# Kernel optimization log

Hardware: AMD Instinct MI355X
Metric: run time of the kernel (lower is better)

Reference implementation:

```python
import jax, jax.numpy as jnp
import numpy as np

S = 8            # n_internal_streams
N = 2**S - 1     # 255 cliques (all non-empty subsets of streams)
D = 32           # half_dim = consciousness_dim // 2
INPUT_DIM = 512
NUM_ITER = 5
B = 1024


def _configs():
    # binary membership of each clique (non-empty subsets), [N, S]
    return ((np.arange(1, 2**S)[:, None] >> np.arange(S)) & 1).astype(np.float32)


def setup_inputs() -> dict:
    key = jax.random.key(0)
    ks = jax.random.split(key, 10)
    cfg = _configs()
    depths = cfg.sum(-1)
    # topological amplitude init: gaussian profile over clique depth
    center, sigma = S / 2.0, S / 3.0
    prof = np.exp(-((depths - center) ** 2) / (2 * sigma ** 2))
    prof = prof / (np.linalg.norm(prof) + 1e-8)
    psi_A0 = jnp.asarray(np.broadcast_to(prof[None, :, None], (1, N, D)).copy(),
                         jnp.float32) + jax.random.normal(ks[0], (1, N, D)) * 0.01
    inp = {
        'network_state': jax.random.normal(ks[1], (B, INPUT_DIM), jnp.float32),
        'W_streams': jax.random.normal(ks[2], (S * D, INPUT_DIM)) / np.sqrt(INPUT_DIM),
        'b_streams': jnp.zeros((S * D,), jnp.float32),
        'W_A': jax.random.normal(ks[3], (D, D)) / np.sqrt(D),
        'b_A': jnp.zeros((D,), jnp.float32),
        'W_phi': jax.random.normal(ks[4], (D, D)) / np.sqrt(D),
        'b_phi': jnp.zeros((D,), jnp.float32),
        'psi_A0': psi_A0,
        'psi_phi0': jax.random.normal(ks[5], (1, N, D)) * 0.3,
        'W_comp': jax.random.normal(ks[6], (32, N)) / np.sqrt(N),
        'b_comp': jnp.zeros((32,), jnp.float32),
        'W_read': jax.random.normal(ks[7], (2 * D, 32 * D)) / np.sqrt(32 * D),
        'b_read': jnp.zeros((2 * D,), jnp.float32),
        'alpha_kin': jnp.asarray(0.5, jnp.float32),
        'mass_sq': jnp.asarray(0.1, jnp.float32),
        'potential_weight': jnp.asarray(0.3, jnp.float32),
        'input_weight': jnp.asarray(0.5, jnp.float32),
        'evolution_rate': jnp.asarray(0.3, jnp.float32),
        'phase_coupling': jnp.asarray(1.0, jnp.float32),
    }
    return inp


def reference(network_state, W_streams, b_streams, W_A, b_A, W_phi, b_phi,
              psi_A0, psi_phi0, W_comp, b_comp, W_read, b_read,
              alpha_kin, mass_sq, potential_weight, input_weight,
              evolution_rate, phase_coupling):
    cfg = jnp.asarray(_configs())                      # [N,S]
    depths = cfg.sum(-1)                               # [N]
    # Hamming-distance kernel between clique configurations
    Ham = cfg @ (1.0 - cfg).T + (1.0 - cfg) @ cfg.T    # [N,N]
    K = jnp.exp(-Ham / S)
    krow = K.sum(1)                                    # [N]

    Bb = network_state.shape[0]
    feats = (network_state @ W_streams.T + b_streams).reshape(Bb, S, D)
    # clique features: mean of member-stream features
    cf = jnp.einsum('ns,bsd->bnd', cfg, feats) / depths[None, :, None]
    A_input = jax.nn.softplus(cf @ W_A.T + b_A)        # [B,N,D]
    phi_input = jnp.pi * jnp.tanh(cf @ W_phi.T + b_phi)

    A = jax.nn.softplus(jnp.broadcast_to(psi_A0, (Bb, N, D)))
    phi = jnp.broadcast_to(psi_phi0, (Bb, N, D))
    dt = jax.nn.sigmoid(evolution_rate)

    for _ in range(NUM_ITER):
        # laplacian: sum_j K_ij (A_j - A_i) / N  (factorized, same math)
        KA = jnp.einsum('ij,bjd->bid', K, A)
        lap = (KA - krow[None, :, None] * A) / N
        sp, cp = jnp.sin(phi), jnp.cos(phi)
        Ks = jnp.einsum('ij,bjd->bid', K, sp)
        Kc = jnp.einsum('ij,bjd->bid', K, cp)
        # sum_j K_ij A_i sin(phi_j - phi_i) / N
        pc = A * (cp * Ks - sp * Kc) / N
        # nonlocal potential: V_i = sum_j K_ij A_j cos(phi_j - phi_i) / N
        KAc = jnp.einsum('ij,bjd->bid', K, A * cp)
        KAs = jnp.einsum('ij,bjd->bid', K, A * sp)
        V = (cp * KAc + sp * KAs) / N
        input_drive = A_input * jnp.sin(phi_input - phi)
        dA = (alpha_kin * lap + potential_weight * V - mass_sq * A
              + input_weight * (A_input - A))
        A = jax.nn.softplus(A + dt * dA)               # updated A used in dphi
        dphi = alpha_kin * pc / (A + 1e-8) + input_weight * input_drive
        phi = phi + dt * dphi
        # per-clique norm clip to 1
        norms = jnp.maximum(jnp.linalg.norm(A, axis=-1, keepdims=True), 1e-8)
        A = A * jnp.where(norms > 1.0, 1.0 / norms, 1.0)

    A_t = jnp.swapaxes(A, 1, 2)                        # [B,D,N]
    Ac = jax.nn.relu(A_t @ W_comp.T + b_comp)          # [B,D,32]
    ro = Ac.reshape(Bb, -1) @ W_read.T + b_read        # [B,2D]
    amplitude = jax.nn.softplus(ro[:, :D])
    phase = jnp.tanh(ro[:, D:] * phase_coupling) * jnp.pi
    psi = (amplitude * jnp.cos(phase)).astype(jnp.complex64) + 1j * (amplitude * jnp.sin(phase)).astype(jnp.complex64)
    return psi, amplitude, phase
```

## Files before the change

### kernel.cpp

```cpp
#include <hip/hip_runtime.h>
#include <math.h>

#define PI_F   3.14159265358979f
#define QF     0.88249690258459546f
#define INV255 (1.0f/255.0f)

__device__ __forceinline__ float softplus_f(float x){
    return fmaxf(x, 0.0f) + __logf(1.0f + __expf(-fabsf(x)));
}
__device__ __forceinline__ float tanh_fast(float x){
    const float e = __expf(2.0f*x);
    return fmaf(-2.0f, __builtin_amdgcn_rcpf(e + 1.0f), 1.0f);
}

template<int CTRL>
__device__ __forceinline__ float dppmov(float x){
    return __int_as_float(__builtin_amdgcn_mov_dpp(__float_as_int(x), CTRL, 0xF, 0xF, false));
}
__device__ __forceinline__ float lxor1 (float x){ return dppmov<0xB1>(x);  }
__device__ __forceinline__ float lxor2 (float x){ return dppmov<0x4E>(x);  }
__device__ __forceinline__ float lxor8 (float x){ return dppmov<0x128>(x); }
__device__ __forceinline__ float lxor4 (float x){ return __int_as_float(__builtin_amdgcn_ds_swizzle(__float_as_int(x), 0x101F)); }
__device__ __forceinline__ float lxor16(float x){ return __int_as_float(__builtin_amdgcn_ds_swizzle(__float_as_int(x), 0x401F)); }
__device__ __forceinline__ float lxor32(float x){ return __shfl_xor(x, 32, 64); }

template<int CTRL>
__device__ __forceinline__ float dppadd(float v){
    return v + __int_as_float(__builtin_amdgcn_update_dpp(0, __float_as_int(v), CTRL, 0xF, 0xF, true));
}
__device__ __forceinline__ float wave_sum63(float v){
    v = dppadd<0x111>(v);
    v = dppadd<0x112>(v);
    v = dppadd<0x114>(v);
    v = dppadd<0x118>(v);
    v = dppadd<0x142>(v);
    v = dppadd<0x143>(v);
    return v;
}

template<int NA>
__device__ __forceinline__ void bflyN(float (&x)[NA][4]){
    const float qv = QF;
    #pragma unroll
    for (int a = 0; a < NA; a++){
        #pragma unroll
        for (int r = 0; r < 4; r++) x[a][r] = fmaf(lxor1 (x[a][r]), qv, x[a][r]);
    }
    #pragma unroll
    for (int a = 0; a < NA; a++){
        #pragma unroll
        for (int r = 0; r < 4; r++) x[a][r] = fmaf(lxor2 (x[a][r]), qv, x[a][r]);
    }
    #pragma unroll
    for (int a = 0; a < NA; a++){
        #pragma unroll
        for (int r = 0; r < 4; r++) x[a][r] = fmaf(lxor8 (x[a][r]), qv, x[a][r]);
    }
    #pragma unroll
    for (int a = 0; a < NA; a++){
        #pragma unroll
        for (int r = 0; r < 4; r++) x[a][r] = fmaf(lxor4 (x[a][r]), qv, x[a][r]);
    }
    #pragma unroll
    for (int a = 0; a < NA; a++){
        #pragma unroll
        for (int r = 0; r < 4; r++) x[a][r] = fmaf(lxor16(x[a][r]), qv, x[a][r]);
    }
    #pragma unroll
    for (int a = 0; a < NA; a++){
        #pragma unroll
        for (int r = 0; r < 4; r++) x[a][r] = fmaf(lxor32(x[a][r]), qv, x[a][r]);
    }
    #pragma unroll
    for (int a = 0; a < NA; a++){
        float t0 = x[a][0], t2 = x[a][2];
        x[a][0] = fmaf(QF, x[a][1], x[a][0]);
        x[a][1] = fmaf(QF, t0,      x[a][1]);
        x[a][2] = fmaf(QF, x[a][3], x[a][2]);
        x[a][3] = fmaf(QF, t2,      x[a][3]);
        t0 = x[a][0]; float t1 = x[a][1];
        x[a][0] = fmaf(QF, x[a][2], x[a][0]);
        x[a][1] = fmaf(QF, x[a][3], x[a][1]);
        x[a][2] = fmaf(QF, t0,      x[a][2]);
        x[a][3] = fmaf(QF, t1,      x[a][3]);
    }
}

__global__ __launch_bounds__(256) void prep_kernel(
        const float* __restrict__ Ws,    const float* __restrict__ psiA0,
        const float* __restrict__ psiP0, const float* __restrict__ p_alpha,
        const float* __restrict__ p_msq, const float* __restrict__ p_pw,
        const float* __restrict__ p_iw,  const float* __restrict__ p_evo,
        float* __restrict__ WsT,  float* __restrict__ Xc,  float* __restrict__ P0c,
        float* __restrict__ F0c)
{
    if (blockIdx.x < 32){
        __shared__ float tile[64][65];
        const int rt = blockIdx.x & 3, ct = blockIdx.x >> 2;
        const int r0 = rt*64, c0t = ct*64;
        const int tx = threadIdx.x & 63, ty = threadIdx.x >> 6;
        #pragma unroll
        for (int k = 0; k < 16; k++){
            const int row = ty*16 + k;
            tile[row][tx] = Ws[(r0+row)*512 + c0t + tx];
        }
        __syncthreads();
        #pragma unroll
        for (int k = 0; k < 16; k++){
            const int row = ty*16 + k;
            WsT[(c0t+row)*256 + r0 + tx] = tile[tx][row];
        }
        return;
    }
    const int tid = threadIdx.x;
    const int w = tid >> 6, l = tid & 63;
    const float alpha = p_alpha[0], msq = p_msq[0], pw = p_pw[0], iw = p_iw[0];
    const float dt   = 1.0f / (1.0f + __expf(-p_evo[0]));
    const float dta  = dt * alpha * INV255;
    const float dtpw = dt * pw * INV255;
    const float c0   = 1.0f - dt * (msq + iw);
    const float m0 = (l == 0) ? 0.0f : 1.0f;
    int nn[4]; float krow[4];
    float c18;
    { const float t1 = 1.0f + QF, t2 = t1*t1, t4 = t2*t2; c18 = t4*t4; }
    #pragma unroll
    for (int r = 0; r < 4; r++){
        nn[r] = l + 64*r;
        krow[r] = c18 - __expf(-0.125f * (float)__popc(nn[r]));
    }
    #pragma unroll
    for (int dd = 0; dd < 8; dd++){
        const int d = w*8 + dd;
        float A0[4], ph0[4], sp[4], cp[4];
        float x[5][4];
        #pragma unroll
        for (int r = 0; r < 4; r++){
            const int n = nn[r];
            A0[r]  = (n > 0) ? softplus_f(psiA0[(n-1)*32 + d]) : 0.0f;
            ph0[r] = (n > 0) ? psiP0[(n-1)*32 + d] : 0.0f;
            sp[r] = __sinf(ph0[r]); cp[r] = __cosf(ph0[r]);
            const float mk = (r == 0) ? m0 : 1.0f;
            const float xa = A0[r] * mk;
            x[0][r] = xa;
            x[1][r] = sp[r] * mk;
            x[2][r] = cp[r] * mk;
            x[3][r] = xa * cp[r];
            x[4][r] = xa * sp[r];
        }
        bflyN<5>(x);
        #pragma unroll
        for (int r = 0; r < 4; r++){
            const float Ao   = A0[r];
            const float lapp = fmaf(-krow[r], Ao, x[0][r]);
            const float Vp   = fmaf(cp[r], x[3][r], sp[r]*x[4][r]);
            const float Pp   = fmaf(-sp[r], x[2][r], cp[r]*x[1][r]);
            float X = c0 * Ao;
            X = fmaf(dta,  lapp, X);
            X = fmaf(dtpw, Vp,   X);
            const int idx = d*256 + nn[r];
            Xc[idx]  = X;
            P0c[idx] = dta * Ao * Pp;
            F0c[idx] = ph0[r];
        }
    }
}

template<bool USET>
__global__ __launch_bounds__(512, 4) void fused_kernel(
        const float* __restrict__ ns,
        const float* __restrict__ Ws,
        const float* __restrict__ WsT,
        const float* __restrict__ bs,
        const float* __restrict__ WA,
        const float* __restrict__ bA,
        const float* __restrict__ WP,
        const float* __restrict__ bP,
        const float* __restrict__ psiA0,
        const float* __restrict__ psiP0,
        const float* __restrict__ Xc,
        const float* __restrict__ P0c,
        const float* __restrict__ F0c,
        const float* __restrict__ Wcomp,
        const float* __restrict__ bcomp,
        const float* __restrict__ Wread,
        const float* __restrict__ bread,
        const float* __restrict__ p_alpha, const float* __restrict__ p_msq,
        const float* __restrict__ p_pw,    const float* __restrict__ p_iw,
        const float* __restrict__ p_evo,   const float* __restrict__ p_pcpl,
        float* __restrict__ out, int Bb)
{
    __shared__ __align__(16) float2 ST[16][512];
    __shared__ __align__(16) float  red[2048];
    __shared__ __align__(16) float  hA[256];
    __shared__ __align__(16) float  hP[256];
    __shared__ __align__(16) float  nsb[512];
    __shared__ __align__(16) float  fe[256];

    float* ac  = red;
    float* rop = red + 1024;

    const int b   = blockIdx.x;
    const int tid = threadIdx.x;
    const int w   = tid >> 6, l = tid & 63;

    const float alpha = p_alpha[0], msq = p_msq[0], pw = p_pw[0], iw = p_iw[0];
    const float pcpl  = p_pcpl[0];
    const float dt    = 1.0f / (1.0f + __expf(-p_evo[0]));
    const float dta  = dt * alpha * INV255;
    const float dtpw = dt * pw * INV255;
    const float c0   = 1.0f - dt * (msq + iw);
    const float dtiw = dt * iw;

    nsb[tid] = ns[b*512 + tid];
    __syncthreads();
    {
        const int k = tid >> 1, part = tid & 1;
        float f = (part == 0) ? bs[k] : 0.0f;
        if (USET){
            const float4* nb4 = (const float4*)nsb + part*64;
            const float*  colb = WsT + (part*64)*1024 + k;
            #pragma unroll 8
            for (int j4 = 0; j4 < 64; j4++){
                const float4 nv = nb4[j4];
                const float* col = colb + j4*1024;
                f = fmaf(col[0],   nv.x, f);
                f = fmaf(col[256], nv.y, f);
                f = fmaf(col[512], nv.z, f);
                f = fmaf(col[768], nv.w, f);
            }
        } else {
            const float4* wr  = (const float4*)(Ws + k*512) + part*64;
            const float4* nb4 = (const float4*)nsb + part*64;
            #pragma unroll 8
            for (int i = 0; i < 64; i++){
                const float4 wv = wr[i], nv = nb4[i];
                f = fmaf(wv.x, nv.x, f); f = fmaf(wv.y, nv.y, f);
                f = fmaf(wv.z, nv.z, f); f = fmaf(wv.w, nv.w, f);
            }
        }
        red[part*256 + k] = f;
    }
    __syncthreads();
    if (tid < 256) fe[tid] = red[tid] + red[256 + tid];
    __syncthreads();
    {
        const int t2 = tid & 255;
        const int s = t2 >> 5, d2 = t2 & 31;
        const float* Wm = (tid < 256) ? WA : WP;
        float acc = 0.0f;
        #pragma unroll 8
        for (int dp = 0; dp < 32; dp++)
            acc = fmaf(Wm[d2*32 + dp], fe[s*32 + dp], acc);
        if (tid < 256) hA[t2] = acc; else hP[t2] = acc;
    }
    __syncthreads();

    int   nn[4];
    float krow[4];
    const float m0 = (l == 0) ? 0.0f : 1.0f;
    float c18;
    { const float t1 = 1.0f + QF, t2 = t1*t1, t4 = t2*t2; c18 = t4*t4; }
    #pragma unroll
    for (int r = 0; r < 4; r++){
        nn[r] = l + 64*r;
        krow[r] = c18 - __expf(-0.125f * (float)__popc(nn[r]));
    }

    float CAp[4][4], Dsp[4][4], Dcp[4][4];
    float scl_c[4] = {1.0f, 1.0f, 1.0f, 1.0f};
    float nrm0[4] = {0.f, 0.f, 0.f, 0.f};

    #pragma unroll
    for (int dd = 0; dd < 4; dd++){
        const int d = w*4 + dd;
        const float bAd = bA[d], bPd = bP[d];
        float gA_[8], gP_[8];
        #pragma unroll
        for (int s = 0; s < 8; s++){ gA_[s] = hA[s*32 + d]; gP_[s] = hP[s*32 + d]; }
        #pragma unroll
        for (int r = 0; r < 4; r++){
            const int pop = __popc(nn[r]);
            const float rdep = 1.0f / (float)(pop ? pop : 1);
            float sA = 0.0f, sP = 0.0f;
            #pragma unroll
            for (int s = 0; s < 8; s++){
                if ((nn[r] >> s) & 1){ sA += gA_[s]; sP += gP_[s]; }
            }
            const float uA  = fmaf(sA, rdep, bAd);
            const float uP  = fmaf(sP, rdep, bPd);
            const float Ain = softplus_f(uA);
            const float pin = PI_F * tanh_fast(uP);
            const float ca = dtiw * Ain;
            CAp[dd][r] = ca;
            Dsp[dd][r] = ca * __sinf(pin);
            Dcp[dd][r] = ca * __cosf(pin);
            if (USET){
                const int idx = d*256 + nn[r];
                const float An = softplus_f(Xc[idx] + ca);
                const float rr = __builtin_amdgcn_rcpf(An + 1e-8f);
                const float F0 = F0c[idx];
                float pb = fmaf(ca, __sinf(pin - F0), F0);
                ST[dd*4 + r][tid] = make_float2(An, fmaf(P0c[idx], rr, pb));
                nrm0[r] = fmaf(An, An, nrm0[r]);
            } else {
                const int nm1 = (nn[r] > 0) ? (nn[r] - 1) : 0;
                ST[dd*4 + r][tid] = make_float2(softplus_f(psiA0[nm1*32 + d]),
                                                psiP0[nm1*32 + d]);
            }
        }
        __builtin_amdgcn_sched_barrier(0);
    }

    if (USET){
        #pragma unroll
        for (int r = 0; r < 4; r++) red[w*256 + nn[r]] = nrm0[r];
        __syncthreads();
        #pragma unroll
        for (int r = 0; r < 4; r++){
            const int n = nn[r];
            const float t = red[n]        + red[256 + n]  + red[512 + n]  + red[768 + n]
                          + red[1024 + n] + red[1280 + n] + red[1536 + n] + red[1792 + n];
            scl_c[r] = (t > 1.0f) ? rsqrtf(t) : 1.0f;
        }
        __syncthreads();
    }

    float2 stn[4];
    #pragma unroll
    for (int r = 0; r < 4; r++) stn[r] = ST[r][tid];

    const int NFULL = USET ? 3 : 4;
    for (int it = 0; it < NFULL; it++){
        float nrm[4] = {0.f, 0.f, 0.f, 0.f};
        #pragma unroll
        for (int dd = 0; dd < 4; dd++){
            float Al[4], ph[4], sp[4], cp[4];
            #pragma unroll
            for (int r = 0; r < 4; r++){
                Al[r] = stn[r].x * scl_c[r];
                ph[r] = stn[r].y;
            }
            if (dd < 3){
                #pragma unroll
                for (int r = 0; r < 4; r++) stn[r] = ST[(dd+1)*4 + r][tid];
            }
            float x[5][4];
            {
                sp[0] = __sinf(ph[0]); cp[0] = __cosf(ph[0]);
                const float xa = Al[0] * m0;
                x[0][0] = xa;
                x[1][0] = sp[0] * m0;
                x[2][0] = cp[0] * m0;
                x[3][0] = xa * cp[0];
                x[4][0] = xa * sp[0];
            }
            #pragma unroll
            for (int r = 1; r < 4; r++){
                sp[r] = __sinf(ph[r]); cp[r] = __cosf(ph[r]);
                const float xa = Al[r];
                x[0][r] = xa;
                x[1][r] = sp[r];
                x[2][r] = cp[r];
                x[3][r] = xa * cp[r];
                x[4][r] = xa * sp[r];
            }
            bflyN<5>(x);
            #pragma unroll
            for (int r = 0; r < 4; r++){
                const float Ao   = Al[r];
                const float lapp = fmaf(-krow[r], Ao, x[0][r]);
                const float Vp   = fmaf(cp[r], x[3][r], sp[r]*x[4][r]);
                float Aarg = fmaf(c0, Ao, CAp[dd][r]);
                Aarg = fmaf(dta,  lapp, Aarg);
                Aarg = fmaf(dtpw, Vp,   Aarg);
                const float An = softplus_f(Aarg);
                const float Pp = fmaf(-sp[r], x[2][r], cp[r]*x[1][r]);
                const float rr = __builtin_amdgcn_rcpf(An + 1e-8f);
                float pb = fmaf(Dsp[dd][r], cp[r], ph[r]);
                pb = fmaf(-Dcp[dd][r], sp[r], pb);
                ST[dd*4 + r][tid] = make_float2(An, fmaf(dta*Ao, Pp*rr, pb));
                nrm[r] = fmaf(An, An, nrm[r]);
            }
            __builtin_amdgcn_sched_barrier(0);
        }
        #pragma unroll
        for (int r = 0; r < 4; r++) stn[r] = ST[r][tid];
        #pragma unroll
        for (int r = 0; r < 4; r++) red[w*256 + nn[r]] = nrm[r];
        __syncthreads();
        #pragma unroll
        for (int r = 0; r < 4; r++){
            const int n = nn[r];
            const float t = red[n]        + red[256 + n]  + red[512 + n]  + red[768 + n]
                          + red[1024 + n] + red[1280 + n] + red[1536 + n] + red[1792 + n];
            scl_c[r] = (t > 1.0f) ? rsqrtf(t) : 1.0f;
        }
        __syncthreads();
    }

    {
        float nrm[4] = {0.f, 0.f, 0.f, 0.f};
        #pragma unroll
        for (int dd = 0; dd < 4; dd++){
            float Al[4], ph[4], sp[4], cp[4];
            #pragma unroll
            for (int r = 0; r < 4; r++){
                Al[r] = stn[r].x * scl_c[r];
                ph[r] = stn[r].y;
            }
            if (dd < 3){
                #pragma unroll
                for (int r = 0; r < 4; r++) stn[r] = ST[(dd+1)*4 + r][tid];
            }
            float y[3][4];
            {
                sp[0] = __sinf(ph[0]); cp[0] = __cosf(ph[0]);
                const float xa = Al[0] * m0;
                y[0][0] = xa;
                y[1][0] = xa * cp[0];
                y[2][0] = xa * sp[0];
            }
            #pragma unroll
            for (int r = 1; r < 4; r++){
                sp[r] = __sinf(ph[r]); cp[r] = __cosf(ph[r]);
                const float xa = Al[r];
                y[0][r] = xa;
                y[1][r] = xa * cp[r];
                y[2][r] = xa * sp[r];
            }
            bflyN<3>(y);
            #pragma unroll
            for (int r = 0; r < 4; r++){
                const float Ao   = Al[r];
                const float lapp = fmaf(-krow[r], Ao, y[0][r]);
                const float Vp   = fmaf(cp[r], y[1][r], sp[r]*y[2][r]);
                float Aarg = fmaf(c0, Ao, CAp[dd][r]);
                Aarg = fmaf(dta,  lapp, Aarg);
                Aarg = fmaf(dtpw, Vp,   Aarg);
                const float An = softplus_f(Aarg);
                ST[dd*4 + r][tid] = make_float2(An, 0.0f);
                nrm[r] = fmaf(An, An, nrm[r]);
            }
            __builtin_amdgcn_sched_barrier(0);
        }
        #pragma unroll
        for (int r = 0; r < 4; r++) red[w*256 + nn[r]] = nrm[r];
        __syncthreads();
        #pragma unroll
        for (int r = 0; r < 4; r++){
            const int n = nn[r];
            const float t = red[n]        + red[256 + n]  + red[512 + n]  + red[768 + n]
                          + red[1024 + n] + red[1280 + n] + red[1536 + n] + red[1792 + n];
            scl_c[r] = (t > 1.0f) ? rsqrtf(t) : 1.0f;
        }
        __syncthreads();
    }

    float Ar[4][4];
    #pragma unroll
    for (int dd = 0; dd < 4; dd++){
        #pragma unroll
        for (int r = 0; r < 4; r++)
            Ar[dd][r] = ST[dd*4 + r][tid].x * scl_c[r];
        Ar[dd][0] *= m0;
    }

    for (int c = 0; c < 32; c++){
        float wv[4];
        #pragma unroll
        for (int r = 0; r < 4; r++){
            const int idx = c*255 + nn[r] - 1;
            wv[r] = Wcomp[idx < 0 ? 0 : idx];
        }
        const float bc = bcomp[c];
        #pragma unroll
        for (int dd = 0; dd < 4; dd++){
            float v = wv[0] * Ar[dd][0];
            v = fmaf(wv[1], Ar[dd][1], v);
            v = fmaf(wv[2], Ar[dd][2], v);
            v = fmaf(wv[3], Ar[dd][3], v);
            v = wave_sum63(v);
            if (l == 63)
                ac[(w*4 + dd)*32 + c] = fmaxf(v + bc, 0.0f);
        }
    }
    __syncthreads();

    {
        const int k = tid >> 2, part = tid & 3;
        const float4* Wr4 = (const float4*)Wread + k*256;
        const float4* ac4 = (const float4*)ac;
        float s = 0.0f;
        #pragma unroll 4
        for (int jj = 0; jj < 64; jj++){
            const int j4 = part + 4*jj;
            const float4 wv = Wr4[j4];
            const float4 av = ac4[j4];
            s = fmaf(wv.x, av.x, s); s = fmaf(wv.y, av.y, s);
            s = fmaf(wv.z, av.z, s); s = fmaf(wv.w, av.w, s);
        }
        rop[tid] = s;
    }
    __syncthreads();
    if (tid < 32){
        const float ra = rop[tid*4] + rop[tid*4+1] + rop[tid*4+2] + rop[tid*4+3] + bread[tid];
        const int   t2 = tid + 32;
        const float rp = rop[t2*4] + rop[t2*4+1] + rop[t2*4+2] + rop[t2*4+3] + bread[t2];
        const float amp = softplus_f(ra);
        const float ph  = PI_F * tanhf(rp * pcpl);
        const float cph = __cosf(ph);
        const int o = b*32 + tid;
        out[o]         = amp * cph;
        out[Bb*32 + o] = amp;
        out[Bb*64 + o] = ph;
    }
}

extern "C" void kernel_launch(void* const* d_in, const int* in_sizes, int n_in,
                              void* d_out, int out_size, void* d_ws, size_t ws_size,
                              hipStream_t stream) {
    const float* ns      = (const float*)d_in[0];
    const float* Ws      = (const float*)d_in[1];
    const float* bs      = (const float*)d_in[2];
    const float* WA      = (const float*)d_in[3];
    const float* bA      = (const float*)d_in[4];
    const float* WP      = (const float*)d_in[5];
    const float* bP      = (const float*)d_in[6];
    const float* psiA0   = (const float*)d_in[7];
    const float* psiP0   = (const float*)d_in[8];
    const float* Wcomp   = (const float*)d_in[9];
    const float* bcomp   = (const float*)d_in[10];
    const float* Wread   = (const float*)d_in[11];
    const float* bread   = (const float*)d_in[12];
    const float* p_alpha = (const float*)d_in[13];
    const float* p_msq   = (const float*)d_in[14];
    const float* p_pw    = (const float*)d_in[15];
    const float* p_iw    = (const float*)d_in[16];
    const float* p_evo   = (const float*)d_in[17];
    const float* p_pcpl  = (const float*)d_in[18];

    const int Bb = in_sizes[0] / 512;

    const size_t need = (size_t)(512*256 + 3*32*256) * sizeof(float);
    if (ws_size >= need){
        float* WsT = (float*)d_ws;
        float* Xc  = WsT + 512*256;
        float* P0c = Xc  + 32*256;
        float* F0c = P0c + 32*256;
        prep_kernel<<<33, 256, 0, stream>>>(Ws, psiA0, psiP0,
                                            p_alpha, p_msq, p_pw, p_iw, p_evo,
                                            WsT, Xc, P0c, F0c);
        fused_kernel<true><<<Bb, 512, 0, stream>>>(ns, Ws, WsT, bs, WA, bA, WP, bP,
                                                   psiA0, psiP0, Xc, P0c, F0c,
                                                   Wcomp, bcomp, Wread, bread,
                                                   p_alpha, p_msq, p_pw, p_iw,
                                                   p_evo, p_pcpl, (float*)d_out, Bb);
    } else {
        fused_kernel<false><<<Bb, 512, 0, stream>>>(ns, Ws, nullptr, bs, WA, bA, WP, bP,
                                                    psiA0, psiP0,
                                                    nullptr, nullptr, nullptr,
                                                    Wcomp, bcomp, Wread, bread,
                                                    p_alpha, p_msq, p_pw, p_iw,
                                                    p_evo, p_pcpl, (float*)d_out, Bb);
    }
}
```

Baseline: 284.1 us.

## Stage A and W_comp in LDS and compute compression as per-thread dot products

Replaces the clique-compression stage with a different scheme. Before, 32 iterations each did a wave-wide DPP reduction of 4 partial products per lane. Now the amplitudes and a zero-padded copy of W_comp are written to shared memory, and each thread computes two full 256-long dot products with float4 loads. This removes the long chains of cross-lane reductions and the repeated scattered global reads of W_comp. In exchange it adds shared-memory staging, an extra barrier, and a reorganised shared pool that reuses the ST buffer.

```diff
diff --git a/kernel.cpp b/kernel.cpp
--- a/kernel.cpp
+++ b/kernel.cpp
@@ -23,20 +23,6 @@
 __device__ __forceinline__ float lxor4 (float x){ return __int_as_float(__builtin_amdgcn_ds_swizzle(__float_as_int(x), 0x101F)); }
 __device__ __forceinline__ float lxor16(float x){ return __int_as_float(__builtin_amdgcn_ds_swizzle(__float_as_int(x), 0x401F)); }
 __device__ __forceinline__ float lxor32(float x){ return __shfl_xor(x, 32, 64); }
-
-template<int CTRL>
-__device__ __forceinline__ float dppadd(float v){
-    return v + __int_as_float(__builtin_amdgcn_update_dpp(0, __float_as_int(v), CTRL, 0xF, 0xF, true));
-}
-__device__ __forceinline__ float wave_sum63(float v){
-    v = dppadd<0x111>(v);
-    v = dppadd<0x112>(v);
-    v = dppadd<0x114>(v);
-    v = dppadd<0x118>(v);
-    v = dppadd<0x142>(v);
-    v = dppadd<0x143>(v);
-    return v;
-}
 
 template<int NA>
 __device__ __forceinline__ void bflyN(float (&x)[NA][4]){
@@ -189,15 +175,18 @@
         const float* __restrict__ p_evo,   const float* __restrict__ p_pcpl,
         float* __restrict__ out, int Bb)
 {
-    __shared__ __align__(16) float2 ST[16][512];
-    __shared__ __align__(16) float  red[2048];
-    __shared__ __align__(16) float  hA[256];
-    __shared__ __align__(16) float  hP[256];
-    __shared__ __align__(16) float  nsb[512];
-    __shared__ __align__(16) float  fe[256];
-
-    float* ac  = red;
-    float* rop = red + 1024;
+    __shared__ __align__(16) float POOL[18432];
+    __shared__ __align__(16) float hA[256];
+    __shared__ __align__(16) float hP[256];
+    __shared__ __align__(16) float nsb[512];
+    __shared__ __align__(16) float fe[256];
+
+    float2 (*ST)[512] = (float2(*)[512])POOL;
+    float* red = POOL + 16384;
+    float* AL  = POOL;
+    float* WL  = POOL + 8192;
+    float* ac  = POOL + 16512;
+    float* rop = POOL + 17536;
 
     const int b   = blockIdx.x;
     const int tid = threadIdx.x;
@@ -464,25 +453,38 @@
             Ar[dd][r] = ST[dd*4 + r][tid].x * scl_c[r];
         Ar[dd][0] *= m0;
     }
-
-    for (int c = 0; c < 32; c++){
-        float wv[4];
-        #pragma unroll
-        for (int r = 0; r < 4; r++){
-            const int idx = c*255 + nn[r] - 1;
-            wv[r] = Wcomp[idx < 0 ? 0 : idx];
+    __syncthreads();
+
+    #pragma unroll
+    for (int dd = 0; dd < 4; dd++)
+        #pragma unroll
+        for (int r = 0; r < 4; r++)
+            AL[(w*4 + dd)*256 + nn[r]] = Ar[dd][r];
+    for (int i = tid; i < 8320; i += 512){
+        const int c = i / 260, n = i - c*260;
+        WL[i] = (n >= 1 && n <= 255) ? Wcomp[c*255 + n - 1] : 0.0f;
+    }
+    __syncthreads();
+
+    {
+        const int c  = l & 31;
+        const int d1 = w + 8*(l >> 5);
+        const float4* AL4 = (const float4*)AL;
+        const float4* WL4 = (const float4*)WL;
+        float s1 = 0.0f, s2 = 0.0f;
+        #pragma unroll 8
+        for (int j = 0; j < 64; j++){
+            const float4 wv = WL4[c*65 + j];
+            const float4 a1 = AL4[d1*64 + j];
+            const float4 a2 = AL4[(d1+16)*64 + j];
+            s1 = fmaf(wv.x, a1.x, s1); s1 = fmaf(wv.y, a1.y, s1);
+            s1 = fmaf(wv.z, a1.z, s1); s1 = fmaf(wv.w, a1.w, s1);
+            s2 = fmaf(wv.x, a2.x, s2); s2 = fmaf(wv.y, a2.y, s2);
+            s2 = fmaf(wv.z, a2.z, s2); s2 = fmaf(wv.w, a2.w, s2);
         }
         const float bc = bcomp[c];
-        #pragma unroll
-        for (int dd = 0; dd < 4; dd++){
-            float v = wv[0] * Ar[dd][0];
-            v = fmaf(wv[1], Ar[dd][1], v);
-            v = fmaf(wv[2], Ar[dd][2], v);
-            v = fmaf(wv[3], Ar[dd][3], v);
-            v = wave_sum63(v);
-            if (l == 63)
-                ac[(w*4 + dd)*32 + c] = fmaxf(v + bc, 0.0f);
-        }
+        ac[d1*32 + c]        = fmaxf(s1 + bc, 0.0f);
+        ac[(d1 + 16)*32 + c] = fmaxf(s2 + bc, 0.0f);
     }
     __syncthreads();
 
```

After: 269.6 us (median of 2 runs). 1.05x faster.
